# Kernel tuning notes

Measured on AMD Instinct MI355X. Metric: run time of the kernel, lower is better.

The kernel has to match this reference:

```python
import jax, jax.numpy as jnp
import numpy as np

N_E, N_U, N_D = 512, 256, 256
N_A = 16
N_FB = 4
N_SV = 256
N_PV = 64
D_IN0 = 3 * (4 * N_A) + 2 * 4   # 200, fb_block output at layer 0
D_IN = 3 * N_SV + 2 * N_PV      # 896, fb_block output thereafter


def _fb_block(s_v, p_v):
    # s_v: (n_e, d_s); p_v: (n_e, n_e, d_p)
    n_e = N_U + N_D
    su_m = jnp.tile(s_v[:N_U].mean(0)[None, :], (n_e, 1))
    sd_m = jnp.tile(s_v[N_U:].mean(0)[None, :], (n_e, 1))
    pu_m = p_v[:N_U].mean(0)   # (n_e, d_p)
    pd_m = p_v[N_U:].mean(0)
    return jnp.concatenate([su_m, sd_m, pu_m, pd_m, s_v], axis=-1)


def setup_inputs() -> dict:
    key = jax.random.key(0)
    ks = jax.random.split(key, 16)

    def lin(k, fin, fout):
        k1, k2 = jax.random.split(k)
        lim = 1.0 / np.sqrt(fin)
        W = jax.random.uniform(k1, (fin, fout), minval=-lim, maxval=lim, dtype=jnp.float32)
        b = jax.random.uniform(k2, (fout,), minval=-lim, maxval=lim, dtype=jnp.float32)
        return W, b

    V0_W, V0_b = lin(ks[0], D_IN0, N_SV)
    W0_W, W0_b = lin(ks[1], 4, N_PV)
    VrW, Vrb, WrW, Wrb = [], [], [], []
    for i in range(N_FB - 1):
        w, b = lin(ks[2 + i], D_IN, N_SV); VrW.append(w); Vrb.append(b)
        w, b = lin(ks[6 + i], N_PV, N_PV); WrW.append(w); Wrb.append(b)
    Vr_W, Vr_b = jnp.stack(VrW), jnp.stack(Vrb)
    Wr_W, Wr_b = jnp.stack(WrW), jnp.stack(Wrb)
    Vhu_W, Vhu_b = lin(ks[10], D_IN, N_SV)
    Vhd_W, Vhd_b = lin(ks[11], D_IN, N_SV)
    wu_W, wu_b = lin(ks[12], N_SV, N_U)
    wd_W, wd_b = lin(ks[13], N_SV, N_D)
    r = jax.random.normal(ks[14], (N_E, 3), dtype=jnp.float32)
    a = jax.random.normal(ks[15], (N_A, 3), dtype=jnp.float32) * 2.0
    return dict(r=r, a=a, V0_W=V0_W, V0_b=V0_b, Vr_W=Vr_W, Vr_b=Vr_b,
                W0_W=W0_W, W0_b=W0_b, Wr_W=Wr_W, Wr_b=Wr_b,
                Vhu_W=Vhu_W, Vhu_b=Vhu_b, Vhd_W=Vhd_W, Vhd_b=Vhd_b,
                wu_W=wu_W, wu_b=wu_b, wd_W=wd_W, wd_b=wd_b)


def reference(r, a, V0_W, V0_b, Vr_W, Vr_b, W0_W, W0_b, Wr_W, Wr_b,
              Vhu_W, Vhu_b, Vhd_W, Vhd_b, wu_W, wu_b, wd_W, wd_b):
    n_e = N_E
    eye = jnp.eye(n_e, dtype=r.dtype)[:, :, None]
    ra = r[:, None, :] - a[None, :, :]                       # (n_e, n_a, 3)
    ra_len = jnp.linalg.norm(ra, axis=-1, keepdims=True)
    rr = r[None, :, :] - r[:, None, :]                       # (n_e, n_e, 3)
    rr_len = jnp.linalg.norm(rr + eye, axis=-1, keepdims=True)
    s_v = jnp.concatenate([ra, ra_len], axis=-1).reshape(n_e, -1)   # (n_e, 4*n_a)
    p_v = jnp.concatenate([rr, rr_len], axis=-1)                    # (n_e, n_e, 4)
    s_blk = _fb_block(s_v, p_v)
    for l in range(N_FB):
        VW, Vb = (V0_W, V0_b) if l == 0 else (Vr_W[l - 1], Vr_b[l - 1])
        WW, Wb = (W0_W, W0_b) if l == 0 else (Wr_W[l - 1], Wr_b[l - 1])
        s_new = jnp.tanh(s_blk @ VW + Vb)
        s_v = s_new + s_v if s_v.shape[-1] == N_SV else s_new   # residual skips layer 0
        p_new = jnp.tanh(p_v @ WW + Wb)
        p_v = p_new + p_v if p_v.shape[-1] == N_PV else p_new
        s_blk = _fb_block(s_v, p_v)
    s_u = jnp.tanh(s_blk[:N_U] @ Vhu_W + Vhu_b)
    s_d = jnp.tanh(s_blk[N_U:] @ Vhd_W + Vhd_b)
    s_wu = s_u @ wu_W + wu_b                                  # (n_u, n_u)
    s_wd = s_d @ wd_W + wd_b                                  # (n_d, n_d)
    exp_u = jnp.linalg.norm(ra[:N_U], axis=-1, keepdims=True)  # (n_u, n_a, 1)
    exp_d = jnp.linalg.norm(ra[N_U:], axis=-1, keepdims=True)
    orb_u = (s_wu * jnp.exp(-exp_u).sum(axis=1))[None]         # (1, n_u, n_u)
    orb_d = (s_wd * jnp.exp(-exp_d).sum(axis=1))[None]
    # logabssumdet with n_det == 1, matrix dim > 1
    sgn_u, log_u = jnp.linalg.slogdet(orb_u)
    sgn_d, log_d = jnp.linalg.slogdet(orb_d)
    psi = (sgn_u * sgn_d * jnp.exp(log_u + log_d)).sum()
    return jnp.log(jnp.abs(psi))
```

## Files before the change

kernel.cpp:

```cpp
#include <hip/hip_runtime.h>
#include <hip/hip_bf16.h>

#define NE 512

__device__ __align__(16) float g_sv0[NE*64];
__device__ __align__(16) float g_sv[2][NE*256];
__device__ __align__(16) float g_pu4[NE*4];
__device__ __align__(16) float g_pd4[NE*4];
__device__ __align__(16) float g_puL[4*NE*64];
__device__ __align__(16) float g_pdL[4*NE*64];
__device__ __align__(16) float g_su0[64];
__device__ __align__(16) float g_sd0[64];
__device__ __align__(16) float g_su[256];
__device__ __align__(16) float g_sd[256];
__device__ __align__(16) float g_part4[4*16*NE*64];
__device__ __align__(16) float g_f[NE];
__device__ __align__(16) float g_hu[256*256];
__device__ __align__(16) float g_hd[256*256];
__device__ __align__(16) float g_orbu[256*256];
__device__ __align__(16) float g_orbd[256*256];
__device__ float g_logs[2];

__device__ __forceinline__ float tanh_fast(float x) {
  float e = __expf(2.f * x);
  return 1.f - 2.f / (e + 1.f);
}

__global__ __launch_bounds__(256, 4) void k_front(const float* __restrict__ r,
                                                  const float* __restrict__ a,
                                                  const float* __restrict__ W0,
                                                  const float* __restrict__ b0,
                                                  const float* __restrict__ Wr,
                                                  const float* __restrict__ brs) {
  __shared__ __align__(16) float xbuf[4][32*64];
  __shared__ float red[4][4];
  int bid = blockIdx.x, t = threadIdx.x;
  if (bid < 512) {
    int j = bid;
    if (j == 0) {
      for (int h = 0; h < 2; ++h) {
        int e = h*256 + t;
        float rx = r[3*e], ry = r[3*e+1], rz = r[3*e+2];
        float facc = 0.f;
        #pragma unroll
        for (int at = 0; at < 16; ++at) {
          float dx = rx - a[3*at], dy = ry - a[3*at+1], dz = rz - a[3*at+2];
          float len = sqrtf(dx*dx + dy*dy + dz*dz);
          g_sv0[e*64 + 4*at + 0] = dx;
          g_sv0[e*64 + 4*at + 1] = dy;
          g_sv0[e*64 + 4*at + 2] = dz;
          g_sv0[e*64 + 4*at + 3] = len;
          facc += expf(-len);
        }
        g_f[e] = facc;
      }
      __syncthreads();
      if (t < 128) {
        int h = t >> 6, c = t & 63;
        float s = 0.f;
        for (int i = 0; i < 256; ++i) s += g_sv0[(h*256 + i)*64 + c];
        (h ? g_sd0 : g_su0)[c] = s * (1.f/256.f);
      }
      __syncthreads();
    }
    float rjx = r[3*j], rjy = r[3*j+1], rjz = r[3*j+2];
    for (int h = 0; h < 2; ++h) {
      int i = h*256 + t;
      float dx = rjx - r[3*i], dy = rjy - r[3*i+1], dz = rjz - r[3*i+2];
      float ee = (i == j) ? 1.f : 0.f;
      float ex = dx+ee, ey = dy+ee, ez = dz+ee;
      float len = sqrtf(ex*ex + ey*ey + ez*ez);
      float v0 = dx, v1 = dy, v2 = dz, v3 = len;
      #pragma unroll
      for (int m = 1; m < 64; m <<= 1) {
        v0 += __shfl_xor(v0, m); v1 += __shfl_xor(v1, m);
        v2 += __shfl_xor(v2, m); v3 += __shfl_xor(v3, m);
      }
      if ((t & 63) == 0) {
        int wv = t >> 6;
        red[wv][0]=v0; red[wv][1]=v1; red[wv][2]=v2; red[wv][3]=v3;
      }
      __syncthreads();
      if (t == 0) {
        float* dst = h ? g_pd4 : g_pu4;
        #pragma unroll
        for (int c = 0; c < 4; ++c)
          dst[j*4 + c] = (red[0][c]+red[1][c]+red[2][c]+red[3][c]) * (1.f/256.f);
      }
      __syncthreads();
    }
  } else {
    int lane = t & 63, wv = t >> 6;
    int gw = (bid - 512)*4 + wv;
    int j = gw >> 4, chunk = gw & 15;
    int i0 = chunk * 32;
    float* xb = xbuf[wv];
    float rjx = r[3*j], rjy = r[3*j+1], rjz = r[3*j+2];
    float macc0 = 0.f, macc1 = 0.f, macc2 = 0.f, macc3 = 0.f;
    {
      float w0 = W0[lane], w1 = W0[64+lane], w2 = W0[128+lane], w3 = W0[192+lane];
      float bb = b0[lane];
      for (int ii = 0; ii < 32; ++ii) {
        int i = i0 + ii;
        float dx = rjx - r[3*i], dy = rjy - r[3*i+1], dz = rjz - r[3*i+2];
        float ee = (i == j) ? 1.f : 0.f;
        float ex = dx+ee, ey = dy+ee, ez = dz+ee;
        float len = sqrtf(ex*ex + ey*ey + ez*ez);
        float y = tanh_fast(bb + dx*w0 + dy*w1 + dz*w2 + len*w3);
        xb[ii*64 + lane] = y;
        macc0 += y;
      }
    }
    for (int l = 0; l < 3; ++l) {
      const float* W = Wr + l*4096;
      float wcol[64];
      #pragma unroll
      for (int k = 0; k < 64; ++k) wcol[k] = W[k*64 + lane];
      float bb = brs[l*64 + lane];
      float mac = 0.f;
      for (int ii = 0; ii < 32; ++ii) {
        const float* row = &xb[ii*64];
        float x = row[lane];
        float acc = bb;
        #pragma unroll
        for (int g = 0; g < 16; ++g) {
          float4 pv = *(const float4*)&row[4*g];
          acc += pv.x*wcol[4*g] + pv.y*wcol[4*g+1] + pv.z*wcol[4*g+2] + pv.w*wcol[4*g+3];
        }
        float y = tanh_fast(acc) + x;
        xb[ii*64 + lane] = y;
        mac += y;
      }
      if (l == 0) macc1 = mac;
      else if (l == 1) macc2 = mac;
      else macc3 = mac;
    }
    int base = chunk*(NE*64) + j*64 + lane;
    g_part4[0*(16*NE*64) + base] = macc0;
    g_part4[1*(16*NE*64) + base] = macc1;
    g_part4[2*(16*NE*64) + base] = macc2;
    g_part4[3*(16*NE*64) + base] = macc3;
  }
}

__global__ __launch_bounds__(256) void k_reduce_p() {
  int idx = blockIdx.x*256 + threadIdx.x;
  int l = idx >> 16;
  int rem = idx & 65535;
  int half = rem >> 15;
  int r2 = rem & 32767;
  int j = r2 >> 6, c = r2 & 63;
  const float* pp = g_part4 + l*(16*NE*64) + half*(8*NE*64) + j*64 + c;
  float s = 0.f;
  #pragma unroll
  for (int ch = 0; ch < 8; ++ch) s += pp[ch*(NE*64)];
  (half ? g_pdL : g_puL)[l*(NE*64) + j*64 + c] = s * (1.f/256.f);
}

__global__ __launch_bounds__(256) void k_smean(int svsel) {
  int h = blockIdx.x, t = threadIdx.x;
  const float* sv = g_sv[svsel];
  float s = 0.f;
  for (int i = 0; i < 256; ++i) s += sv[(h*256 + i)*256 + t];
  (h ? g_sd : g_su)[t] = s * (1.f/256.f);
}

template<int PUK, int SVK, int MEANK>
__global__ __launch_bounds__(256) void k_smm(int which, const float* __restrict__ W,
                                             const float* __restrict__ Wb,
                                             const float* __restrict__ W2,
                                             const float* __restrict__ Wb2,
                                             int pl) {
  constexpr int MAINK = 2*PUK + SVK;
  __shared__ __align__(16) float wsl[MAINK*32];
  __shared__ float insl[32*(MAINK+1)];
  __shared__ float biasv[32];
  __shared__ float bred[256];
  const float *pu_p=nullptr, *pd_p=nullptr, *sv_p=nullptr, *su_p=nullptr, *sd_p=nullptr;
  const float *res_p=nullptr, *rs_p=nullptr;
  float* out_p = nullptr;
  int t = threadIdx.x;
  int rg = blockIdx.x, cg = blockIdx.y;
  int grp = 0, rgl = rg;
  if (which >= 4) { grp = rg >> 3; rgl = rg & 7; }
  const float* Wsel = (which >= 4 && grp) ? W2 : W;
  const float* Wbsel = (which >= 4 && grp) ? Wb2 : Wb;
  int in_base = 0, dotanh = 1;
  switch (which) {
    case 0: pu_p=g_pu4; pd_p=g_pd4; su_p=g_su0; sd_p=g_sd0; sv_p=g_sv0;
            out_p=g_sv[0]; in_base=rg*32; break;
    case 1: case 2: case 3:
      pu_p=g_puL + pl*(NE*64); pd_p=g_pdL + pl*(NE*64); su_p=g_su; sd_p=g_sd;
      sv_p=g_sv[(which+1)&1]; res_p=sv_p; out_p=g_sv[which&1]; in_base=rg*32; break;
    case 4: pu_p=g_puL + pl*(NE*64); pd_p=g_pdL + pl*(NE*64); su_p=g_su; sd_p=g_sd;
            sv_p=g_sv[1]; out_p = grp ? g_hd : g_hu; in_base = grp*256 + rgl*32; break;
    default: sv_p = grp ? g_hd : g_hu; out_p = grp ? g_orbd : g_orbu;
             rs_p = g_f + grp*256; in_base = rgl*32; dotanh = 0; break;
  }
  int out_base = (which >= 4) ? rgl*32 : rg*32;
  int col0 = cg * 32;
  for (int idx = t; idx < MAINK*32; idx += 256) {
    int c = idx >> 5, cl = idx & 31;
    wsl[idx] = Wsel[(2*MEANK + c)*256 + col0 + cl];
  }
  for (int rr = 0; rr < 32; ++rr) {
    int row = in_base + rr;
    for (int c = t; c < MAINK; c += 256) {
      float v;
      if (c < PUK) v = pu_p[row*PUK + c];
      else if (c < 2*PUK) v = pd_p[row*PUK + (c - PUK)];
      else v = sv_p[row*SVK + (c - 2*PUK)];
      insl[rr*(MAINK+1) + c] = v;
    }
  }
  {
    int pcol = t & 31, ps = t >> 5;
    float bacc = 0.f;
    if (MEANK > 0) {
      for (int c = ps; c < MEANK; c += 8)
        bacc += su_p[c]*Wsel[c*256 + col0 + pcol] + sd_p[c]*Wsel[(MEANK + c)*256 + col0 + pcol];
    }
    bred[ps*32 + pcol] = bacc;
  }
  __syncthreads();
  if (t < 32) {
    float s = Wbsel[col0 + t];
    #pragma unroll
    for (int p8 = 0; p8 < 8; ++p8) s += bred[p8*32 + t];
    biasv[t] = s;
  }
  __syncthreads();
  int c4 = t & 7, rl = t >> 3;
  float a0 = biasv[4*c4], a1 = biasv[4*c4+1], a2 = biasv[4*c4+2], a3 = biasv[4*c4+3];
  const float* inrow = &insl[rl*(MAINK+1)];
  #pragma unroll 4
  for (int c = 0; c < MAINK; ++c) {
    float iv = inrow[c];
    float4 wv = *(const float4*)&wsl[c*32 + 4*c4];
    a0 += iv*wv.x; a1 += iv*wv.y; a2 += iv*wv.z; a3 += iv*wv.w;
  }
  int rowA = out_base + rl;
  int col = col0 + 4*c4;
  if (dotanh) { a0=tanh_fast(a0); a1=tanh_fast(a1); a2=tanh_fast(a2); a3=tanh_fast(a3); }
  if (res_p) {
    float4 rv = *(const float4*)&res_p[rowA*256 + col];
    a0 += rv.x; a1 += rv.y; a2 += rv.z; a3 += rv.w;
  }
  if (rs_p) { float fsc = rs_p[rowA]; a0*=fsc; a1*=fsc; a2*=fsc; a3*=fsc; }
  float4 ov; ov.x=a0; ov.y=a1; ov.z=a2; ov.w=a3;
  *(float4*)&out_p[rowA*256 + col] = ov;
}

#define REP8(M) M(0) M(1) M(2) M(3) M(4) M(5) M(6) M(7)
#define DPPMAX(v, CTRL) { unsigned _o = (unsigned)__builtin_amdgcn_update_dpp(0, (int)(v), CTRL, 0xf, 0xf, true); \
                          (v) = (v) > _o ? (v) : _o; }

__global__ __launch_bounds__(512, 2) void k_lu() {
  __shared__ __align__(16) float colbuf[2][256];
  __shared__ __align__(16) float prowbuf[2][16*20];
  const float* A = (blockIdx.x == 0) ? g_orbu : g_orbd;
  int t = threadIdx.x;
  int tile_c = t >> 5;
  int tile_r = t & 31;
  int lane = t & 63;
  int br = tile_r * 8;
  int pb = tile_c * 20;
  const float4* Ap = (const float4*)(A + br*256 + tile_c*16);
#define DECLROW(R) float4 M##R##_0 = Ap[R*64+0], M##R##_1 = Ap[R*64+1], \
                          M##R##_2 = Ap[R*64+2], M##R##_3 = Ap[R*64+3];
  REP8(DECLROW)
#undef DECLROW
  unsigned um = 0;
  if (tile_c == 0) {
#define INIT0(R) colbuf[0][br+R] = M##R##_0.x;
    REP8(INIT0)
#undef INIT0
  }
  __syncthreads();
  float prod = 1.f;
  int esum = 0;
  float m0=0,m1=0,m2=0,m3=0,m4=0,m5=0,m6=0,m7=0;
  for (int k = 0; k < 256; ++k) {
    const float* cbin = colbuf[k & 1];
    float4 cv = *(const float4*)&cbin[4*lane];
    float4 ca = *(const float4*)&cbin[br];
    float4 cb2 = *(const float4*)&cbin[br+4];
    bool aliveU = (tile_c*16 + 15) >= k;
    if (k > 0 && aliveU) {
      const float* pwp = &prowbuf[(k-1) & 1][pb];
      float4 P0 = *(const float4*)&pwp[0];
      float4 P1 = *(const float4*)&pwp[4];
      float4 P2 = *(const float4*)&pwp[8];
      float4 P3 = *(const float4*)&pwp[12];
#define UPD(R) { float mr = m##R; \
  M##R##_0.x -= mr*P0.x; M##R##_0.y -= mr*P0.y; M##R##_0.z -= mr*P0.z; M##R##_0.w -= mr*P0.w; \
  M##R##_1.x -= mr*P1.x; M##R##_1.y -= mr*P1.y; M##R##_1.z -= mr*P1.z; M##R##_1.w -= mr*P1.w; \
  M##R##_2.x -= mr*P2.x; M##R##_2.y -= mr*P2.y; M##R##_2.z -= mr*P2.z; M##R##_2.w -= mr*P2.w; \
  M##R##_3.x -= mr*P3.x; M##R##_3.y -= mr*P3.y; M##R##_3.z -= mr*P3.z; M##R##_3.w -= mr*P3.w; }
      REP8(UPD)
#undef UPD
    }
    unsigned b0 = (um & 1u) ? 0u : ((__float_as_uint(fabsf(cv.x)) & 0xFFFFFF00u) | (unsigned)(4*lane+0));
    unsigned b1 = (um & 2u) ? 0u : ((__float_as_uint(fabsf(cv.y)) & 0xFFFFFF00u) | (unsigned)(4*lane+1));
    unsigned b2 = (um & 4u) ? 0u : ((__float_as_uint(fabsf(cv.z)) & 0xFFFFFF00u) | (unsigned)(4*lane+2));
    unsigned b3 = (um & 8u) ? 0u : ((__float_as_uint(fabsf(cv.w)) & 0xFFFFFF00u) | (unsigned)(4*lane+3));
    unsigned bb = max(max(b0,b1), max(b2,b3));
    DPPMAX(bb, 0x111) DPPMAX(bb, 0x112) DPPMAX(bb, 0x114) DPPMAX(bb, 0x118)
    DPPMAX(bb, 0x142) DPPMAX(bb, 0x143)
    bb = (unsigned)__builtin_amdgcn_readlane((int)bb, 63);
    int p = (int)(bb & 255u);
    int wl = p >> 2, cc = p & 3;
    unsigned px = (unsigned)__builtin_amdgcn_readlane((int)__float_as_uint(cv.x), wl);
    unsigned py = (unsigned)__builtin_amdgcn_readlane((int)__float_as_uint(cv.y), wl);
    unsigned pz = (unsigned)__builtin_amdgcn_readlane((int)__float_as_uint(cv.z), wl);
    unsigned pw = (unsigned)__builtin_amdgcn_readlane((int)__float_as_uint(cv.w), wl);
    float piv = __uint_as_float(cc==0 ? px : cc==1 ? py : cc==2 ? pz : pw);
    int ee; float mant = frexpf(fabsf(piv), &ee);
    prod *= mant; esum += ee;
    int e2; prod = frexpf(prod, &e2); esum += e2;
    if (wl == lane) um |= 1u << cc;
    if (k == 255) break;
    float rp = 1.0f / piv;
    m0 = ca.x*rp; m1 = ca.y*rp; m2 = ca.z*rp; m3 = ca.w*rp;
    m4 = cb2.x*rp; m5 = cb2.y*rp; m6 = cb2.z*rp; m7 = cb2.w*rp;
    bool aliveK = (tile_c*16 + 15) > k;
    if (aliveK && tile_r == (p >> 3)) {
      float* pw_ = &prowbuf[k & 1][pb];
      switch (p & 7) {
#define PUBC(R) case R: *(float4*)&pw_[0] = M##R##_0; *(float4*)&pw_[4] = M##R##_1; \
                        *(float4*)&pw_[8] = M##R##_2; *(float4*)&pw_[12] = M##R##_3; break;
        REP8(PUBC)
#undef PUBC
      }
    }
    int kn = k + 1;
    if (tile_c == (kn >> 4)) {
      float e0,e1,e2b,e3,e4,e5,e6,e7;
      switch (kn & 15) {
#define EXTC(I, G, C) case I: e0=M0_##G.C; e1=M1_##G.C; e2b=M2_##G.C; e3=M3_##G.C; \
                              e4=M4_##G.C; e5=M5_##G.C; e6=M6_##G.C; e7=M7_##G.C; break;
        EXTC(0,0,x) EXTC(1,0,y) EXTC(2,0,z) EXTC(3,0,w)
        EXTC(4,1,x) EXTC(5,1,y) EXTC(6,1,z) EXTC(7,1,w)
        EXTC(8,2,x) EXTC(9,2,y) EXTC(10,2,z) EXTC(11,2,w)
        EXTC(12,3,x) EXTC(13,3,y) EXTC(14,3,z) EXTC(15,3,w)
#undef EXTC
      }
      float sel;
      switch (p & 7) {
        case 0: sel = e0; break; case 1: sel = e1; break;
        case 2: sel = e2b; break; case 3: sel = e3; break;
        case 4: sel = e4; break; case 5: sel = e5; break;
        case 6: sel = e6; break; default: sel = e7; break;
      }
      float pv = __shfl(sel, (tile_c & 1)*32 + (p >> 3), 64);
      float4 w0, w1;
      w0.x = e0 - m0*pv; w0.y = e1 - m1*pv; w0.z = e2b - m2*pv; w0.w = e3 - m3*pv;
      w1.x = e4 - m4*pv; w1.y = e5 - m5*pv; w1.z = e6 - m6*pv; w1.w = e7 - m7*pv;
      *(float4*)&colbuf[kn & 1][br] = w0;
      *(float4*)&colbuf[kn & 1][br+4] = w1;
    }
    __syncthreads();
  }
  if (t == 0) g_logs[blockIdx.x] = logf(prod) + (float)esum * 0.69314718055994531f;
}

__global__ void k_final(float* out) { out[0] = g_logs[0] + g_logs[1]; }

extern "C" void kernel_launch(void* const* d_in, const int* in_sizes, int n_in,
                              void* d_out, int out_size, void* d_ws, size_t ws_size,
                              hipStream_t stream) {
  const float* r     = (const float*)d_in[0];
  const float* a     = (const float*)d_in[1];
  const float* V0_W  = (const float*)d_in[2];
  const float* V0_b  = (const float*)d_in[3];
  const float* Vr_W  = (const float*)d_in[4];
  const float* Vr_b  = (const float*)d_in[5];
  const float* W0_W  = (const float*)d_in[6];
  const float* W0_b  = (const float*)d_in[7];
  const float* Wr_W  = (const float*)d_in[8];
  const float* Wr_b  = (const float*)d_in[9];
  const float* Vhu_W = (const float*)d_in[10];
  const float* Vhu_b = (const float*)d_in[11];
  const float* Vhd_W = (const float*)d_in[12];
  const float* Vhd_b = (const float*)d_in[13];
  const float* wu_W  = (const float*)d_in[14];
  const float* wu_b  = (const float*)d_in[15];
  const float* wd_W  = (const float*)d_in[16];
  const float* wd_b  = (const float*)d_in[17];
  float* out = (float*)d_out;

  k_front<<<2560, 256, 0, stream>>>(r, a, W0_W, W0_b, Wr_W, Wr_b);
  k_reduce_p<<<1024, 256, 0, stream>>>();

  k_smm<4,64,64><<<dim3(16,8), 256, 0, stream>>>(0, V0_W, V0_b, nullptr, nullptr, 0);
  k_smean<<<2, 256, 0, stream>>>(0);
  k_smm<64,256,256><<<dim3(16,8), 256, 0, stream>>>(1, Vr_W + 0*896*256, Vr_b + 0,
                                                    nullptr, nullptr, 0);
  k_smean<<<2, 256, 0, stream>>>(1);
  k_smm<64,256,256><<<dim3(16,8), 256, 0, stream>>>(2, Vr_W + 1*896*256, Vr_b + 256,
                                                    nullptr, nullptr, 1);
  k_smean<<<2, 256, 0, stream>>>(0);
  k_smm<64,256,256><<<dim3(16,8), 256, 0, stream>>>(3, Vr_W + 2*896*256, Vr_b + 512,
                                                    nullptr, nullptr, 2);
  k_smean<<<2, 256, 0, stream>>>(1);
  k_smm<64,256,256><<<dim3(16,8), 256, 0, stream>>>(4, Vhu_W, Vhu_b, Vhd_W, Vhd_b, 3);
  k_smm<0,256,0><<<dim3(16,8), 256, 0, stream>>>(6, wu_W, wu_b, wd_W, wd_b, 0);
  k_lu<<<2, 512, 0, stream>>>();
  k_final<<<1, 1, 0, stream>>>(out);
}
```

Measured before the change: 640.7 us.

## Register-tile the pair-feature MLP and stage layer weights in shared memory

```diff
diff --git a/kernel.cpp b/kernel.cpp
--- a/kernel.cpp
+++ b/kernel.cpp
@@ -26,13 +26,15 @@
   return 1.f - 2.f / (e + 1.f);
 }
 
-__global__ __launch_bounds__(256, 4) void k_front(const float* __restrict__ r,
+__global__ __launch_bounds__(256, 2) void k_front(const float* __restrict__ r,
                                                   const float* __restrict__ a,
                                                   const float* __restrict__ W0,
                                                   const float* __restrict__ b0,
                                                   const float* __restrict__ Wr,
                                                   const float* __restrict__ brs) {
-  __shared__ __align__(16) float xbuf[4][32*64];
+  __shared__ __align__(16) float xrow[4*32*68];
+  __shared__ __align__(16) float wtile[4096];
+  __shared__ __align__(16) float msc[4*4*68];
   __shared__ float red[4][4];
   int bid = blockIdx.x, t = threadIdx.x;
   if (bid < 512) {
@@ -94,52 +96,81 @@
     int gw = (bid - 512)*4 + wv;
     int j = gw >> 4, chunk = gw & 15;
     int i0 = chunk * 32;
-    float* xb = xbuf[wv];
+    int rg = lane >> 4, cg = lane & 15;
+    float* xr = xrow + wv*(32*68);
+    float* ms = msc + wv*(4*68);
     float rjx = r[3*j], rjy = r[3*j+1], rjz = r[3*j+2];
-    float macc0 = 0.f, macc1 = 0.f, macc2 = 0.f, macc3 = 0.f;
+    float xres[8][4];
     {
-      float w0 = W0[lane], w1 = W0[64+lane], w2 = W0[128+lane], w3 = W0[192+lane];
-      float bb = b0[lane];
-      for (int ii = 0; ii < 32; ++ii) {
-        int i = i0 + ii;
+      float4 w0 = *(const float4*)&W0[0*64 + 4*cg];
+      float4 w1 = *(const float4*)&W0[1*64 + 4*cg];
+      float4 w2 = *(const float4*)&W0[2*64 + 4*cg];
+      float4 w3 = *(const float4*)&W0[3*64 + 4*cg];
+      float4 bv = *(const float4*)&b0[4*cg];
+      #pragma unroll
+      for (int q = 0; q < 8; ++q) {
+        int row = 4*q + rg;
+        int i = i0 + row;
         float dx = rjx - r[3*i], dy = rjy - r[3*i+1], dz = rjz - r[3*i+2];
         float ee = (i == j) ? 1.f : 0.f;
         float ex = dx+ee, ey = dy+ee, ez = dz+ee;
         float len = sqrtf(ex*ex + ey*ey + ez*ez);
-        float y = tanh_fast(bb + dx*w0 + dy*w1 + dz*w2 + len*w3);
-        xb[ii*64 + lane] = y;
-        macc0 += y;
-      }
+        float y0 = tanh_fast(bv.x + dx*w0.x + dy*w1.x + dz*w2.x + len*w3.x);
+        float y1 = tanh_fast(bv.y + dx*w0.y + dy*w1.y + dz*w2.y + len*w3.y);
+        float y2 = tanh_fast(bv.z + dx*w0.z + dy*w1.z + dz*w2.z + len*w3.z);
+        float y3 = tanh_fast(bv.w + dx*w0.w + dy*w1.w + dz*w2.w + len*w3.w);
+        xres[q][0]=y0; xres[q][1]=y1; xres[q][2]=y2; xres[q][3]=y3;
+        float4 yv; yv.x=y0; yv.y=y1; yv.z=y2; yv.w=y3;
+        *(float4*)&xr[row*68 + 4*cg] = yv;
+      }
+      float cs0=0,cs1=0,cs2=0,cs3=0;
+      #pragma unroll
+      for (int q=0;q<8;++q){cs0+=xres[q][0];cs1+=xres[q][1];cs2+=xres[q][2];cs3+=xres[q][3];}
+      ms[rg*68+4*cg+0]=cs0; ms[rg*68+4*cg+1]=cs1;
+      ms[rg*68+4*cg+2]=cs2; ms[rg*68+4*cg+3]=cs3;
+      float tot = ms[0*68+lane]+ms[1*68+lane]+ms[2*68+lane]+ms[3*68+lane];
+      g_part4[0*(16*NE*64) + chunk*(NE*64) + j*64 + lane] = tot;
     }
     for (int l = 0; l < 3; ++l) {
-      const float* W = Wr + l*4096;
-      float wcol[64];
+      __syncthreads();
+      for (int idx = t; idx < 4096; idx += 256) wtile[idx] = Wr[l*4096 + idx];
+      __syncthreads();
+      float4 bv = *(const float4*)&brs[l*64 + 4*cg];
+      float acc[8][4];
       #pragma unroll
-      for (int k = 0; k < 64; ++k) wcol[k] = W[k*64 + lane];
-      float bb = brs[l*64 + lane];
-      float mac = 0.f;
-      for (int ii = 0; ii < 32; ++ii) {
-        const float* row = &xb[ii*64];
-        float x = row[lane];
-        float acc = bb;
+      for (int q=0;q<8;++q){acc[q][0]=bv.x;acc[q][1]=bv.y;acc[q][2]=bv.z;acc[q][3]=bv.w;}
+      #pragma unroll 4
+      for (int kq = 0; kq < 16; ++kq) {
+        float4 wv0 = *(const float4*)&wtile[(4*kq+0)*64 + 4*cg];
+        float4 wv1 = *(const float4*)&wtile[(4*kq+1)*64 + 4*cg];
+        float4 wv2 = *(const float4*)&wtile[(4*kq+2)*64 + 4*cg];
+        float4 wv3 = *(const float4*)&wtile[(4*kq+3)*64 + 4*cg];
         #pragma unroll
-        for (int g = 0; g < 16; ++g) {
-          float4 pv = *(const float4*)&row[4*g];
-          acc += pv.x*wcol[4*g] + pv.y*wcol[4*g+1] + pv.z*wcol[4*g+2] + pv.w*wcol[4*g+3];
+        for (int q = 0; q < 8; ++q) {
+          float4 xv = *(const float4*)&xr[(4*q+rg)*68 + 4*kq];
+          acc[q][0] += xv.x*wv0.x + xv.y*wv1.x + xv.z*wv2.x + xv.w*wv3.x;
+          acc[q][1] += xv.x*wv0.y + xv.y*wv1.y + xv.z*wv2.y + xv.w*wv3.y;
+          acc[q][2] += xv.x*wv0.z + xv.y*wv1.z + xv.z*wv2.z + xv.w*wv3.z;
+          acc[q][3] += xv.x*wv0.w + xv.y*wv1.w + xv.z*wv2.w + xv.w*wv3.w;
         }
-        float y = tanh_fast(acc) + x;
-        xb[ii*64 + lane] = y;
-        mac += y;
-      }
-      if (l == 0) macc1 = mac;
-      else if (l == 1) macc2 = mac;
-      else macc3 = mac;
-    }
-    int base = chunk*(NE*64) + j*64 + lane;
-    g_part4[0*(16*NE*64) + base] = macc0;
-    g_part4[1*(16*NE*64) + base] = macc1;
-    g_part4[2*(16*NE*64) + base] = macc2;
-    g_part4[3*(16*NE*64) + base] = macc3;
+      }
+      float cs0=0,cs1=0,cs2=0,cs3=0;
+      #pragma unroll
+      for (int q = 0; q < 8; ++q) {
+        float y0 = tanh_fast(acc[q][0]) + xres[q][0];
+        float y1 = tanh_fast(acc[q][1]) + xres[q][1];
+        float y2 = tanh_fast(acc[q][2]) + xres[q][2];
+        float y3 = tanh_fast(acc[q][3]) + xres[q][3];
+        xres[q][0]=y0; xres[q][1]=y1; xres[q][2]=y2; xres[q][3]=y3;
+        float4 yv; yv.x=y0; yv.y=y1; yv.z=y2; yv.w=y3;
+        *(float4*)&xr[(4*q+rg)*68 + 4*cg] = yv;
+        cs0+=y0; cs1+=y1; cs2+=y2; cs3+=y3;
+      }
+      ms[rg*68+4*cg+0]=cs0; ms[rg*68+4*cg+1]=cs1;
+      ms[rg*68+4*cg+2]=cs2; ms[rg*68+4*cg+3]=cs3;
+      float tot = ms[0*68+lane]+ms[1*68+lane]+ms[2*68+lane]+ms[3*68+lane];
+      g_part4[(l+1)*(16*NE*64) + chunk*(NE*64) + j*64 + lane] = tot;
+    }
   }
 }
 
```

Result: no change. 641.8 us (+0.2%).
